# Performance work log

Measured on AMD Instinct MI355X. Metric: run time of the kernel, lower is better.

The kernel has to match this reference:

```python
import jax, jax.numpy as jnp
import numpy as np

N_PAIRS = 64000
N_ATOMS = 16000
N_PAIR_FEATURES = 8
N_HIDDEN = 100


def setup_inputs() -> dict:
    key = jax.random.key(0)
    k1, k2, k3, k4 = jax.random.split(key, 4)
    pair_features = jax.random.normal(k1, (N_PAIRS, N_PAIR_FEATURES), dtype=jnp.float32)
    atom_features = jax.random.normal(k2, (N_ATOMS, N_HIDDEN), dtype=jnp.float32)
    atom_to_pair = jax.random.randint(k3, (N_PAIRS, 2), 0, N_ATOMS, dtype=jnp.int32)
    W = jax.random.normal(k4, (N_PAIR_FEATURES, N_HIDDEN * N_HIDDEN), dtype=jnp.float32) * 0.1
    b = jnp.zeros((N_HIDDEN * N_HIDDEN,), dtype=jnp.float32)
    return {"pair_features": pair_features, "atom_features": atom_features,
            "atom_to_pair": atom_to_pair, "W": W, "b": b}


def reference(pair_features, atom_features, atom_to_pair, W, b):
    n_atoms, n_hidden = atom_features.shape
    # Dense projection: [E, F] @ [F, H*H] -> per-edge HxH matrices
    A = (pair_features @ W + b).reshape(-1, n_hidden, n_hidden)  # [E, H, H]
    # Gather source-atom features (column 1 of atom_to_pair)
    src = atom_features[atom_to_pair[:, 1]]                      # [E, H]
    # Batched matrix-vector multiply per edge
    msg = jnp.einsum('eij,ej->ei', A, src)                       # [E, H]
    # Scatter-reduce messages onto destination atoms (column 0)
    return jax.ops.segment_sum(msg, atom_to_pair[:, 0], num_segments=n_atoms)
```

## Files before the change

### kernel.cpp

```cpp
#include <hip/hip_runtime.h>
#include <hip/hip_bf16.h>

#define N_PAIRS   64000
#define N_ATOMS   16000
#define N_FEAT    8
#define N_HIDDEN  100
#define SW        1024
#define SKL       936
#define MAX_DEG   32

#define SETUP_BLOCKS (112 * 1024 / 256)
#define HIST_BLOCKS  (N_PAIRS / 256)

typedef __attribute__((ext_vector_type(8))) short bf16x8_t;
typedef __attribute__((ext_vector_type(4))) float f32x4_t;

__global__ __launch_bounds__(256) void setup_hist(const float* __restrict__ W,
                                                  const float* __restrict__ b,
                                                  const int* __restrict__ a2p,
                                                  __hip_bfloat16* __restrict__ wtb2,
                                                  int* __restrict__ deg,
                                                  unsigned* __restrict__ bucket) {
    int bid = blockIdx.x;
    if (bid < SETUP_BLOCKS) {
        int id = bid * 256 + threadIdx.x;
        int i = id >> 10;
        int k = id & 1023;
        float v = 0.f;
        if (i < N_HIDDEN) {
            if (k < 800) {
                int f = k / N_HIDDEN;
                int j = k - f * N_HIDDEN;
                v = W[f * (N_HIDDEN * N_HIDDEN) + i * N_HIDDEN + j];
            } else if (k < 900) {
                int j = k - 800;
                v = b[i * N_HIDDEN + j];
            }
        }
        wtb2[id] = __float2bfloat16(v);
    } else {
        int e = (bid - SETUP_BLOCKS) * 256 + threadIdx.x;
        int dest = a2p[e * 2];
        int src  = a2p[e * 2 + 1];
        int slot = atomicAdd(&deg[dest], 1);
        if (slot < MAX_DEG)
            bucket[dest * MAX_DEG + slot] = ((unsigned)e << 14) | (unsigned)src;
    }
}

__global__ __launch_bounds__(512) void fused_edge_gemm(const float* __restrict__ af,
                                                       const float* __restrict__ pf,
                                                       const int* __restrict__ deg,
                                                       const unsigned* __restrict__ bucket,
                                                       const __hip_bfloat16* __restrict__ wtb2,
                                                       float* __restrict__ out) {
    __shared__ __hip_bfloat16 St[16 * SKL];
    int blk  = blockIdx.x;
    int wave = threadIdx.x >> 6;
    int lane = threadIdx.x & 63;
    bool act = (lane < 50);

#pragma unroll
    for (int j = 0; j < 2; ++j) {
        int r = wave * 2 + j;
        int d = __builtin_amdgcn_readfirstlane(blk * 16 + r);
        int n = deg[d];
        if (n > MAX_DEG) n = MAX_DEG;

        const unsigned* sb = bucket + (size_t)d * MAX_DEG;

        float acc[9][2] = {};
        for (int t0 = 0; t0 < n; t0 += 4) {
            float2 a[4];
            unsigned pk[4];
#pragma unroll
            for (int u = 0; u < 4; ++u) {
                int t = t0 + u;
                pk[u] = sb[t < n ? t : 0];
                int src = (int)(pk[u] & 16383u);
                if (t < n && act)
                    a[u] = *(const float2*)(af + src * N_HIDDEN + 2 * lane);
                else
                    a[u] = make_float2(0.f, 0.f);
            }
#pragma unroll
            for (int u = 0; u < 4; ++u) {
                int e = (int)(pk[u] >> 14);
                const float* pe = pf + e * N_FEAT;
#pragma unroll
                for (int f = 0; f < N_FEAT; ++f) {
                    float p = pe[f];
                    acc[f][0] += p * a[u].x;
                    acc[f][1] += p * a[u].y;
                }
                acc[8][0] += a[u].x;
                acc[8][1] += a[u].y;
            }
        }

        __hip_bfloat16* srow = St + r * SKL;
        if (act) {
#pragma unroll
            for (int f = 0; f < 9; ++f) {
                __hip_bfloat162 h;
                h.x = __float2bfloat16(acc[f][0]);
                h.y = __float2bfloat16(acc[f][1]);
                *(__hip_bfloat162*)(srow + f * N_HIDDEN + 2 * lane) = h;
            }
        } else if (lane < 64) {
            __hip_bfloat162 z;
            z.x = __float2bfloat16(0.f);
            z.y = z.x;
            *(__hip_bfloat162*)(srow + 900 + 2 * (lane - 50)) = z;
        }
    }
    __syncthreads();

    if (wave < 7) {
        int quad = lane >> 4;
        int l15  = lane & 15;
        int m0   = blk * 16;
        const __hip_bfloat16* as = St + l15 * SKL + quad * 8;
        const __hip_bfloat16* bp = wtb2 + (size_t)(wave * 16 + l15) * SW + quad * 8;
        f32x4_t accd = {0.f, 0.f, 0.f, 0.f};
#pragma unroll
        for (int k = 0; k < 29; ++k) {
            bf16x8_t aa = *(const bf16x8_t*)(as + k * 32);
            bf16x8_t bb = *(const bf16x8_t*)(bp + k * 32);
            accd = __builtin_amdgcn_mfma_f32_16x16x32_bf16(aa, bb, accd, 0, 0, 0);
        }
        int c = wave * 16 + l15;
        if (c < N_HIDDEN) {
#pragma unroll
            for (int rr = 0; rr < 4; ++rr)
                out[(size_t)(m0 + quad * 4 + rr) * N_HIDDEN + c] = accd[rr];
        }
    }
}

extern "C" void kernel_launch(void* const* d_in, const int* in_sizes, int n_in,
                              void* d_out, int out_size, void* d_ws, size_t ws_size,
                              hipStream_t stream) {
    const float* pf  = (const float*)d_in[0];
    const float* af  = (const float*)d_in[1];
    const int*   a2p = (const int*)d_in[2];
    const float* W   = (const float*)d_in[3];
    const float* b   = (const float*)d_in[4];
    float* out = (float*)d_out;

    char* ws = (char*)d_ws;
    __hip_bfloat16* wtb2 = (__hip_bfloat16*)ws;
    int* deg             = (int*)(ws + 229376);
    unsigned* bucket     = (unsigned*)(ws + 229376 + 64000);

    hipMemsetAsync(deg, 0, N_ATOMS * sizeof(int), stream);
    setup_hist<<<SETUP_BLOCKS + HIST_BLOCKS, 256, 0, stream>>>(W, b, a2p, wtb2, deg, bucket);
    fused_edge_gemm<<<N_ATOMS / 16, 512, 0, stream>>>(af, pf, deg, bucket, wtb2, out);
}
```

Baseline: 103.3 us.

## Merge memset, setup and edge GEMM into one cooperative kernel with grid syncs

```diff
diff --git a/kernel.cpp b/kernel.cpp
--- a/kernel.cpp
+++ b/kernel.cpp
@@ -1,5 +1,8 @@
 #include <hip/hip_runtime.h>
 #include <hip/hip_bf16.h>
+#include <hip/hip_cooperative_groups.h>
+
+namespace cg = cooperative_groups;
 
 #define N_PAIRS   64000
 #define N_ATOMS   16000
@@ -9,11 +12,145 @@
 #define SKL       936
 #define MAX_DEG   32
 
+#define GRID_B    500
+#define TPB       512
+#define TILES_PER_BLOCK 2
+
 #define SETUP_BLOCKS (112 * 1024 / 256)
 #define HIST_BLOCKS  (N_PAIRS / 256)
 
 typedef __attribute__((ext_vector_type(8))) short bf16x8_t;
 typedef __attribute__((ext_vector_type(4))) float f32x4_t;
+
+__global__ __launch_bounds__(TPB, 4) void mega(const float* __restrict__ pf,
+                                               const float* __restrict__ af,
+                                               const int* __restrict__ a2p,
+                                               const float* __restrict__ W,
+                                               const float* __restrict__ bias,
+                                               __hip_bfloat16* __restrict__ wtb2,
+                                               int* __restrict__ deg,
+                                               unsigned* __restrict__ bucket,
+                                               float* __restrict__ out) {
+    cg::grid_group gg = cg::this_grid();
+    __shared__ __hip_bfloat16 St[16 * SKL];
+    const int tid  = threadIdx.x;
+    const int gtid = blockIdx.x * TPB + tid;
+
+    if (gtid < N_ATOMS) atomicExch(&deg[gtid], 0);
+    if (gtid < 112 * 1024) {
+        int i = gtid >> 10;
+        int k = gtid & 1023;
+        float v = 0.f;
+        if (i < N_HIDDEN) {
+            if (k < 800) {
+                int f = k / N_HIDDEN;
+                int j = k - f * N_HIDDEN;
+                v = W[f * (N_HIDDEN * N_HIDDEN) + i * N_HIDDEN + j];
+            } else if (k < 900) {
+                v = bias[i * N_HIDDEN + (k - 800)];
+            }
+        }
+        wtb2[gtid] = __float2bfloat16(v);
+    }
+    __threadfence();
+    gg.sync();
+
+    if (gtid < N_PAIRS) {
+        int dest = a2p[gtid * 2];
+        int src  = a2p[gtid * 2 + 1];
+        int slot = atomicAdd(&deg[dest], 1);
+        if (slot < MAX_DEG)
+            bucket[dest * MAX_DEG + slot] = ((unsigned)gtid << 14) | (unsigned)src;
+    }
+    __threadfence();
+    gg.sync();
+
+    const int wave = tid >> 6;
+    const int lane = tid & 63;
+    const bool act = (lane < 50);
+
+    for (int it = 0; it < TILES_PER_BLOCK; ++it) {
+        const int tile = blockIdx.x + GRID_B * it;
+
+#pragma unroll
+        for (int j = 0; j < 2; ++j) {
+            int r = wave * 2 + j;
+            int d = __builtin_amdgcn_readfirstlane(tile * 16 + r);
+            int n = deg[d];
+            if (n > MAX_DEG) n = MAX_DEG;
+
+            const unsigned* sb = bucket + (size_t)d * MAX_DEG;
+
+            float acc[9][2] = {};
+            for (int t0 = 0; t0 < n; t0 += 4) {
+                float2 a[4];
+                unsigned pk[4];
+#pragma unroll
+                for (int u = 0; u < 4; ++u) {
+                    int t = t0 + u;
+                    pk[u] = sb[t < n ? t : 0];
+                    int src = (int)(pk[u] & 16383u);
+                    if (t < n && act)
+                        a[u] = *(const float2*)(af + src * N_HIDDEN + 2 * lane);
+                    else
+                        a[u] = make_float2(0.f, 0.f);
+                }
+#pragma unroll
+                for (int u = 0; u < 4; ++u) {
+                    int e = (int)(pk[u] >> 14);
+                    const float* pe = pf + e * N_FEAT;
+#pragma unroll
+                    for (int f = 0; f < N_FEAT; ++f) {
+                        float p = pe[f];
+                        acc[f][0] += p * a[u].x;
+                        acc[f][1] += p * a[u].y;
+                    }
+                    acc[8][0] += a[u].x;
+                    acc[8][1] += a[u].y;
+                }
+            }
+
+            __hip_bfloat16* srow = St + r * SKL;
+            if (act) {
+#pragma unroll
+                for (int f = 0; f < 9; ++f) {
+                    __hip_bfloat162 h;
+                    h.x = __float2bfloat16(acc[f][0]);
+                    h.y = __float2bfloat16(acc[f][1]);
+                    *(__hip_bfloat162*)(srow + f * N_HIDDEN + 2 * lane) = h;
+                }
+            } else {
+                __hip_bfloat162 z;
+                z.x = __float2bfloat16(0.f);
+                z.y = z.x;
+                *(__hip_bfloat162*)(srow + 900 + 2 * (lane - 50)) = z;
+            }
+        }
+        __syncthreads();
+
+        if (wave < 7) {
+            int quad = lane >> 4;
+            int l15  = lane & 15;
+            int m0   = tile * 16;
+            const __hip_bfloat16* as = St + l15 * SKL + quad * 8;
+            const __hip_bfloat16* bp = wtb2 + (size_t)(wave * 16 + l15) * SW + quad * 8;
+            f32x4_t accd = {0.f, 0.f, 0.f, 0.f};
+#pragma unroll
+            for (int k = 0; k < 29; ++k) {
+                bf16x8_t aa = *(const bf16x8_t*)(as + k * 32);
+                bf16x8_t bb = *(const bf16x8_t*)(bp + k * 32);
+                accd = __builtin_amdgcn_mfma_f32_16x16x32_bf16(aa, bb, accd, 0, 0, 0);
+            }
+            int c = wave * 16 + l15;
+            if (c < N_HIDDEN) {
+#pragma unroll
+                for (int rr = 0; rr < 4; ++rr)
+                    out[(size_t)(m0 + quad * 4 + rr) * N_HIDDEN + c] = accd[rr];
+            }
+        }
+        __syncthreads();
+    }
+}
 
 __global__ __launch_bounds__(256) void setup_hist(const float* __restrict__ W,
                                                   const float* __restrict__ b,
@@ -33,8 +170,7 @@
                 int j = k - f * N_HIDDEN;
                 v = W[f * (N_HIDDEN * N_HIDDEN) + i * N_HIDDEN + j];
             } else if (k < 900) {
-                int j = k - 800;
-                v = b[i * N_HIDDEN + j];
+                v = b[i * N_HIDDEN + (k - 800)];
             }
         }
         wtb2[id] = __float2bfloat16(v);
@@ -66,9 +202,7 @@
         int d = __builtin_amdgcn_readfirstlane(blk * 16 + r);
         int n = deg[d];
         if (n > MAX_DEG) n = MAX_DEG;
-
         const unsigned* sb = bucket + (size_t)d * MAX_DEG;
-
         float acc[9][2] = {};
         for (int t0 = 0; t0 < n; t0 += 4) {
             float2 a[4];
@@ -97,7 +231,6 @@
                 acc[8][1] += a[u].y;
             }
         }
-
         __hip_bfloat16* srow = St + r * SKL;
         if (act) {
 #pragma unroll
@@ -107,7 +240,7 @@
                 h.y = __float2bfloat16(acc[f][1]);
                 *(__hip_bfloat162*)(srow + f * N_HIDDEN + 2 * lane) = h;
             }
-        } else if (lane < 64) {
+        } else {
             __hip_bfloat162 z;
             z.x = __float2bfloat16(0.f);
             z.y = z.x;
@@ -153,7 +286,13 @@
     int* deg             = (int*)(ws + 229376);
     unsigned* bucket     = (unsigned*)(ws + 229376 + 64000);
 
-    hipMemsetAsync(deg, 0, N_ATOMS * sizeof(int), stream);
-    setup_hist<<<SETUP_BLOCKS + HIST_BLOCKS, 256, 0, stream>>>(W, b, a2p, wtb2, deg, bucket);
-    fused_edge_gemm<<<N_ATOMS / 16, 512, 0, stream>>>(af, pf, deg, bucket, wtb2, out);
-}
+    void* args[] = {(void*)&pf, (void*)&af, (void*)&a2p, (void*)&W, (void*)&b,
+                    (void*)&wtb2, (void*)&deg, (void*)&bucket, (void*)&out};
+    hipError_t err = hipLaunchCooperativeKernel((const void*)mega, dim3(GRID_B),
+                                                dim3(TPB), args, 0, stream);
+    if (err != hipSuccess) {
+        hipMemsetAsync(deg, 0, N_ATOMS * sizeof(int), stream);
+        setup_hist<<<SETUP_BLOCKS + HIST_BLOCKS, 256, 0, stream>>>(W, b, a2p, wtb2, deg, bucket);
+        fused_edge_gemm<<<N_ATOMS / 16, 512, 0, stream>>>(af, pf, deg, bucket, wtb2, out);
+    }
+}
```

New measurement: 332.3 us. 222% more time.
